# Optimization experiments

Hardware: AMD Instinct MI355X
Metric: run time of the kernel (lower is better)

Reference implementation:

```python
import jax, jax.numpy as jnp
import numpy as np

B, P, V, L = 256, 512, 8, 16
N = B * P            # 131072 nodes
C = V * L            # 128 in_channels (== out_channels, forced by the .view in forward)
H = 4                # heads
DOUT = 128           # out_channels per head
E = N * 5            # k=5 neighbors per node
NEG_SLOPE = 0.2


def setup_inputs() -> dict:
    key = jax.random.key(0)
    ks = jax.random.split(key, 8)
    patches = jax.random.normal(ks[0], (B, P, V, L), dtype=jnp.float32)
    edge_index = jax.random.randint(ks[1], (2, E), 0, N, dtype=jnp.int64)
    s = 1.0 / np.sqrt(C)
    W_gat = jax.random.uniform(ks[2], (C, H * DOUT), dtype=jnp.float32, minval=-s, maxval=s)
    att_src = jax.random.uniform(ks[3], (H, DOUT), dtype=jnp.float32, minval=-s, maxval=s)
    att_dst = jax.random.uniform(ks[4], (H, DOUT), dtype=jnp.float32, minval=-s, maxval=s)
    bias_gat = jnp.zeros((H * DOUT,), dtype=jnp.float32)
    s2 = 1.0 / np.sqrt(H * DOUT)
    W_lin = jax.random.uniform(ks[5], (H * DOUT, DOUT), dtype=jnp.float32, minval=-s2, maxval=s2)
    b_lin = jax.random.uniform(ks[6], (DOUT,), dtype=jnp.float32, minval=-s2, maxval=s2)
    return {"patches": patches, "edge_index": edge_index, "W_gat": W_gat,
            "att_src": att_src, "att_dst": att_dst, "bias_gat": bias_gat,
            "W_lin": W_lin, "b_lin": b_lin}


def reference(patches, edge_index, W_gat, att_src, att_dst, bias_gat, W_lin, b_lin):
    b, p, v, l = patches.shape
    n = b * p
    x = patches.reshape(n, v * l)                      # [N, C]
    xw = (x @ W_gat).reshape(n, H, DOUT)               # [N, H, D]
    # PyG GATConv default add_self_loops=True
    loops = jnp.arange(n, dtype=edge_index.dtype)
    src = jnp.concatenate([edge_index[0], loops])      # message source j
    dst = jnp.concatenate([edge_index[1], loops])      # message target i
    a_src = jnp.einsum('nhd,hd->nh', xw, att_src)      # [N, H]
    a_dst = jnp.einsum('nhd,hd->nh', xw, att_dst)
    e = jax.nn.leaky_relu(a_src[src] + a_dst[dst], NEG_SLOPE)   # [Etot, H]
    m = jax.ops.segment_max(e, dst, num_segments=n)
    ex = jnp.exp(e - m[dst])
    denom = jax.ops.segment_sum(ex, dst, num_segments=n)
    alpha = ex / (denom[dst] + 1e-16)                  # segment softmax over in-edges
    out = jax.ops.segment_sum(alpha[:, :, None] * xw[src], dst, num_segments=n)  # [N, H, D]
    out = out.reshape(n, H * DOUT) + bias_gat
    out = jax.nn.elu(out)
    out = out @ W_lin + b_lin                          # [N, DOUT]
    return out.reshape(b, p, v, l)
```

## Files before the change

### kernel.cpp

```cpp
#include <hip/hip_runtime.h>
#include <hip/hip_bf16.h>
#include <stdint.h>

#define N_NODES 131072
#define C_IN    128
#define HEADS   4
#define DHEAD   128
#define HD      512
#define E_EDGES 655360
#define NEG_SLOPE 0.2f
#define NCHUNK  4
#define CHUNK_N (N_NODES / NCHUNK)
#define SCAN_B  (N_NODES / 256)

typedef short bf16x8 __attribute__((ext_vector_type(8)));
typedef float f32x4  __attribute__((ext_vector_type(4)));

__device__ __forceinline__ float bf2f(unsigned short u) {
    unsigned int x = ((unsigned int)u) << 16;
    return __builtin_bit_cast(float, x);
}
__device__ __forceinline__ unsigned short f2bf(float f) {
    unsigned int u = __builtin_bit_cast(unsigned int, f);
    unsigned int r = u + 0x7FFFu + ((u >> 16) & 1u);
    return (unsigned short)(r >> 16);
}
__device__ __forceinline__ float lrelu(float v) {
    return v > 0.0f ? v : NEG_SLOPE * v;
}

__global__ void detect_kernel(const unsigned int* p_f, const unsigned int* p_i, int* flags) {
    int lane = threadIdx.x;
    int cnt = 0;
#pragma unroll
    for (int r = 0; r < 4; r++) {
        unsigned int e = (p_f[lane + 64 * r] >> 7) & 0xFFu;
        cnt += (e >= 110u && e <= 137u) ? 1 : 0;
    }
    int z = 0;
#pragma unroll
    for (int r = 0; r < 2; r++) {
        z += (p_i[2 * (lane + 64 * r) + 1] == 0u) ? 1 : 0;
    }
#pragma unroll
    for (int o = 1; o < 64; o <<= 1) {
        cnt += __shfl_xor(cnt, o, 64);
        z   += __shfl_xor(z, o, 64);
    }
    if (lane == 0) {
        flags[0] = (cnt >= 128) ? 1 : 0;
        flags[1] = (z == 128) ? 1 : 0;
    }
}

__global__ void conv_w1(const void* in, unsigned short* out, const int* flags) {
    int idx = blockIdx.x * blockDim.x + threadIdx.x;
    int e = idx & 7;
    int l = (idx >> 3) & 63;
    int t = idx >> 9;
    int kk = t & 3, g = t >> 2;
    int col = g * 16 + (l & 15);
    int k = kk * 32 + (l >> 4) * 8 + e;
    float v = flags[0] ? bf2f(((const unsigned short*)in)[k * HD + col])
                       : ((const float*)in)[k * HD + col];
    out[idx] = f2bf(v);
}

__global__ void conv_w2(const void* in, unsigned short* out, const int* flags) {
    int idx = blockIdx.x * blockDim.x + threadIdx.x;
    int n = idx >> 9, k = idx & 511;
    float v = flags[0] ? bf2f(((const unsigned short*)in)[k * DHEAD + n])
                       : ((const float*)in)[k * DHEAD + n];
    out[idx] = f2bf(v);
}

__global__ void conv_small(const void* as, const void* ad, const void* bg, const void* bl,
                           float* att_s, float* att_d, float* bias_g, float* b_lin,
                           const int* flags) {
    int i = blockIdx.x * blockDim.x + threadIdx.x;
    bool bf = flags[0] != 0;
    if (i < 512) {
        att_s[i] = bf ? bf2f(((const unsigned short*)as)[i]) : ((const float*)as)[i];
    } else if (i < 1024) {
        int j = i - 512;
        att_d[j] = bf ? bf2f(((const unsigned short*)ad)[j]) : ((const float*)ad)[j];
    } else if (i < 1536) {
        int j = i - 1024;
        bias_g[j] = bf ? bf2f(((const unsigned short*)bg)[j]) : ((const float*)bg)[j];
    } else if (i < 1664) {
        int j = i - 1536;
        b_lin[j] = bf ? bf2f(((const unsigned short*)bl)[j]) : ((const float*)bl)[j];
    }
}

__global__ void conv_edges_hist(const void* in, int* src32, int* dst32, int* deg,
                                const int* flags) {
    int i = blockIdx.x * blockDim.x + threadIdx.x;
    if (i >= 2 * E_EDGES) return;
    int v = flags[1] ? (int)((const long long*)in)[i] : ((const int*)in)[i];
    if (i < E_EDGES) {
        src32[i] = v;
    } else {
        dst32[i - E_EDGES] = v;
        atomicAdd(&deg[v], 1);
    }
}

__global__ void zero_deg(int* deg) {
    int i = blockIdx.x * blockDim.x + threadIdx.x;
    deg[i] = 0;
}

__global__ void scan_local(const int* __restrict__ deg, int* __restrict__ offv,
                           int* __restrict__ bsums) {
    __shared__ int tmp[256];
    int t = threadIdx.x;
    int g = blockIdx.x * 256 + t;
    int v = deg[g];
    tmp[t] = v;
    __syncthreads();
#pragma unroll
    for (int d = 1; d < 256; d <<= 1) {
        int x = (t >= d) ? tmp[t - d] : 0;
        __syncthreads();
        tmp[t] += x;
        __syncthreads();
    }
    offv[g] = tmp[t] - v;
    if (t == 255) bsums[blockIdx.x] = tmp[t];
}

__global__ void scan_bsums(int* bsums) {
    __shared__ int tmp[SCAN_B];
    int t = threadIdx.x;
    int v = bsums[t];
    tmp[t] = v;
    __syncthreads();
#pragma unroll
    for (int d = 1; d < SCAN_B; d <<= 1) {
        int x = (t >= d) ? tmp[t - d] : 0;
        __syncthreads();
        tmp[t] += x;
        __syncthreads();
    }
    bsums[t] = tmp[t] - v;
}

__global__ void scan_apply(int* __restrict__ offv, const int* __restrict__ bsums,
                           int* __restrict__ cursor) {
    int g = blockIdx.x * 256 + threadIdx.x;
    int v = offv[g] + bsums[blockIdx.x];
    offv[g] = v;
    cursor[g] = v;
}

__global__ void scatter_kernel(const int* src32, const int* dst32, int* cursor, int* csr) {
    int i = blockIdx.x * blockDim.x + threadIdx.x;
    int d = dst32[i];
    int pos = atomicAdd(&cursor[d], 1);
    csr[pos] = src32[i];
}

__launch_bounds__(256)
__global__ void gemm1_fused(const void* __restrict__ Ain,
                            const unsigned short* __restrict__ BT2,
                            const float* __restrict__ attS, const float* __restrict__ attD,
                            unsigned short* __restrict__ xw,
                            float* __restrict__ aSrc, float* __restrict__ aDst,
                            const int* __restrict__ flags) {
    __shared__ unsigned short lA[128 * 136];
    int tid = threadIdx.x;
    int m0 = blockIdx.x * 128;

    if (flags[0] == 0) {
        const float* Af = (const float*)Ain;
#pragma unroll
        for (int p = 0; p < 16; p++) {
            int l = p * 256 + tid;
            int r = l >> 5, c = (l & 31) * 4;
            float4 f = *(const float4*)&Af[(size_t)(m0 + r) * C_IN + c];
            unsigned short t4[4] = {f2bf(f.x), f2bf(f.y), f2bf(f.z), f2bf(f.w)};
            *(uint2*)&lA[r * 136 + c] = *(const uint2*)t4;
        }
    } else {
        const unsigned short* Ab = (const unsigned short*)Ain;
#pragma unroll
        for (int p = 0; p < 8; p++) {
            int l = p * 256 + tid;
            int r = l >> 4, c = (l & 15) * 8;
            *(uint4*)&lA[r * 136 + c] = *(const uint4*)&Ab[(size_t)(m0 + r) * C_IN + c];
        }
    }
    __syncthreads();

    int w = tid >> 6, lane = tid & 63;
    int lr = lane & 15, half = lane >> 4;

    const float4* attS4 = (const float4*)attS;
    const float4* attD4 = (const float4*)attD;

    float dS[8], dD[8];
#pragma unroll
    for (int i = 0; i < 8; i++) { dS[i] = 0.f; dD[i] = 0.f; }

    bf16x8 bbuf[2][4];
#pragma unroll
    for (int kk = 0; kk < 4; kk++)
        bbuf[0][kk] = *(const bf16x8*)&BT2[(((w * 8 + 0) * 4 + kk) << 9) + (lane << 3)];

#pragma unroll
    for (int p = 0; p < 8; p++) {
        int cur = p & 1;
        if (p < 7) {
#pragma unroll
            for (int kk = 0; kk < 4; kk++)
                bbuf[cur ^ 1][kk] =
                    *(const bf16x8*)&BT2[(((w * 8 + p + 1) * 4 + kk) << 9) + (lane << 3)];
        }

        f32x4 acc[8];
#pragma unroll
        for (int i = 0; i < 8; i++) acc[i] = (f32x4){0.f, 0.f, 0.f, 0.f};

#pragma unroll
        for (int kk = 0; kk < 4; kk++) {
#pragma unroll
            for (int i = 0; i < 8; i++) {
                bf16x8 af = *(const bf16x8*)&lA[(i * 16 + lr) * 136 + kk * 32 + half * 8];
                acc[i] = __builtin_amdgcn_mfma_f32_16x16x32_bf16(bbuf[cur][kk], af, acc[i], 0, 0, 0);
            }
        }

        float4 s4 = attS4[w * 32 + p * 4 + half];
        float4 d4 = attD4[w * 32 + p * 4 + half];
#pragma unroll
        for (int i = 0; i < 8; i++) {
            dS[i] += acc[i][0] * s4.x + acc[i][1] * s4.y + acc[i][2] * s4.z + acc[i][3] * s4.w;
            dD[i] += acc[i][0] * d4.x + acc[i][1] * d4.y + acc[i][2] * d4.z + acc[i][3] * d4.w;
            uint2 pk;
            pk.x = (unsigned int)f2bf(acc[i][0]) | ((unsigned int)f2bf(acc[i][1]) << 16);
            pk.y = (unsigned int)f2bf(acc[i][2]) | ((unsigned int)f2bf(acc[i][3]) << 16);
            *(uint2*)&xw[(size_t)(m0 + i * 16 + lr) * HD + w * 128 + p * 16 + half * 4] = pk;
        }
    }

#pragma unroll
    for (int i = 0; i < 8; i++) {
        float ps = dS[i], pd = dD[i];
        ps += __shfl_xor(ps, 16, 64);
        ps += __shfl_xor(ps, 32, 64);
        pd += __shfl_xor(pd, 16, 64);
        pd += __shfl_xor(pd, 32, 64);
        if (half == 0) {
            aSrc[(size_t)(m0 + i * 16 + lr) * HEADS + w] = ps;
            aDst[(size_t)(m0 + i * 16 + lr) * HEADS + w] = pd;
        }
    }
}

__launch_bounds__(256)
__global__ void gemm2(const unsigned short* __restrict__ A,
                      const unsigned short* __restrict__ BT,
                      const float* __restrict__ bias,
                      unsigned short* Cbf, float* Cf,
                      const int* __restrict__ flags, long long rowOff) {
    __shared__ unsigned short smem[64 * 136];
    unsigned short* lA = smem;
    unsigned short* lB = smem + 64 * 40;
    int tid = threadIdx.x;
    int m0 = blockIdx.x * 64;
    int wid = tid >> 6, lane = tid & 63;
    int wr = (wid >> 1) * 32, wc = (wid & 1) * 64;
    int lr = lane & 15, half = lane >> 4;

    f32x4 acc[2][4];
#pragma unroll
    for (int i = 0; i < 2; i++)
#pragma unroll
        for (int j = 0; j < 4; j++) acc[i][j] = (f32x4){0.f, 0.f, 0.f, 0.f};

    for (int k0 = 0; k0 < HD; k0 += 32) {
        {
            int r = tid >> 2, c = (tid & 3) * 8;
            *(uint4*)&lA[r * 40 + c] = *(const uint4*)&A[(size_t)(m0 + r) * HD + k0 + c];
        }
#pragma unroll
        for (int p = 0; p < 2; p++) {
            int l = p * 256 + tid;
            int r = l >> 2, c = (l & 3) * 8;
            *(uint4*)&lB[r * 40 + c] = *(const uint4*)&BT[(size_t)r * HD + k0 + c];
        }
        __syncthreads();
        bf16x8 af[2], bfr[4];
#pragma unroll
        for (int i = 0; i < 2; i++)
            af[i] = *(const bf16x8*)&lA[(wr + i * 16 + lr) * 40 + half * 8];
#pragma unroll
        for (int j = 0; j < 4; j++)
            bfr[j] = *(const bf16x8*)&lB[(wc + j * 16 + lr) * 40 + half * 8];
#pragma unroll
        for (int i = 0; i < 2; i++)
#pragma unroll
            for (int j = 0; j < 4; j++)
                acc[i][j] = __builtin_amdgcn_mfma_f32_16x16x32_bf16(af[i], bfr[j], acc[i][j], 0, 0, 0);
        __syncthreads();
    }

    if (flags[0] != 0) {
#pragma unroll
        for (int i = 0; i < 2; i++)
#pragma unroll
            for (int j = 0; j < 4; j++) {
                int gcol = wc + j * 16 + lr;
                float b = bias[gcol];
#pragma unroll
                for (int r = 0; r < 4; r++)
                    smem[(wr + i * 16 + half * 4 + r) * 136 + gcol] = f2bf(acc[i][j][r] + b);
            }
        __syncthreads();
#pragma unroll
        for (int p = 0; p < 2; p++) {
            int l = p * 256 + tid;
            int r = l >> 4, c = (l & 15) * 8;
            *(uint4*)&Cbf[(size_t)(rowOff + m0 + r) * DHEAD + c] = *(const uint4*)&smem[r * 136 + c];
        }
    } else {
#pragma unroll
        for (int i = 0; i < 2; i++)
#pragma unroll
            for (int j = 0; j < 4; j++) {
                int gcol = wc + j * 16 + lr;
                float b = bias[gcol];
#pragma unroll
                for (int r = 0; r < 4; r++) {
                    int grow = m0 + wr + i * 16 + half * 4 + r;
                    Cf[(size_t)(rowOff + grow) * DHEAD + gcol] = acc[i][j][r] + b;
                }
            }
    }
}

__launch_bounds__(256)
__global__ void aggregate(const unsigned short* __restrict__ xw,
                          const float* __restrict__ a_src, const float* __restrict__ a_dst,
                          const int* __restrict__ off, const int* __restrict__ deg,
                          const int* __restrict__ csr, const float* __restrict__ bias_g,
                          unsigned short* __restrict__ y, int nodeBase) {
    int local = blockIdx.x * 4 + (threadIdx.x >> 6);
    int node = nodeBase + local;
    int l = threadIdx.x & 63;
    int h = l >> 4;
    int ebase = l * 8;
    int o = off[node], dn = deg[node];
    float ad = a_dst[node * HEADS + h];

    float acc[8];
    float denom;
    {
        float w = __expf(lrelu(a_src[node * HEADS + h] + ad));
        uint4 q = *(const uint4*)&xw[(size_t)node * HD + ebase];
        const unsigned short* u = (const unsigned short*)&q;
        denom = w;
#pragma unroll
        for (int k = 0; k < 8; k++) acc[k] = w * bf2f(u[k]);
    }

    for (int e0 = 0; e0 < dn; e0 += 8) {
        int   idx[8];
        float as[8];
        uint4 px[8];
#pragma unroll
        for (int b = 0; b < 8; b++)
            idx[b] = (e0 + b < dn) ? csr[o + e0 + b] : node;
#pragma unroll
        for (int b = 0; b < 8; b++)
            as[b] = a_src[idx[b] * HEADS + h];
#pragma unroll
        for (int b = 0; b < 8; b++)
            px[b] = *(const uint4*)&xw[(size_t)idx[b] * HD + ebase];
#pragma unroll
        for (int b = 0; b < 8; b++) {
            float w = (e0 + b < dn) ? __expf(lrelu(as[b] + ad)) : 0.0f;
            denom += w;
            const unsigned short* u = (const unsigned short*)&px[b];
#pragma unroll
            for (int k = 0; k < 8; k++) acc[k] += w * bf2f(u[k]);
        }
    }

    float inv = 1.0f / (denom + 1e-16f);
    unsigned short outp[8];
#pragma unroll
    for (int k = 0; k < 8; k++) {
        float v = acc[k] * inv + bias_g[ebase + k];
        v = v > 0.f ? v : (__expf(v) - 1.0f);
        outp[k] = f2bf(v);
    }
    *(uint4*)&y[(size_t)local * HD + ebase] = *(const uint4*)outp;
}

extern "C" void kernel_launch(void* const* d_in, const int* in_sizes, int n_in,
                              void* d_out, int out_size, void* d_ws, size_t ws_size,
                              hipStream_t stream) {
    char* ws = (char*)d_ws;
    size_t wsoff = 0;
    auto alloc = [&](size_t bytes) -> char* {
        char* p = ws + wsoff;
        wsoff += (bytes + 255) & ~(size_t)255;
        return p;
    };

    int*            flags  = (int*)           alloc(256);
    unsigned short* WT1    = (unsigned short*)alloc((size_t)HD * C_IN * 2);
    unsigned short* WT2    = (unsigned short*)alloc((size_t)DHEAD * HD * 2);
    float*          attS   = (float*)         alloc(HD * 4);
    float*          attD   = (float*)         alloc(HD * 4);
    float*          biasG  = (float*)         alloc(HD * 4);
    float*          bLin   = (float*)         alloc(DHEAD * 4);
    int*            src32  = (int*)           alloc((size_t)E_EDGES * 4);
    int*            dst32  = (int*)           alloc((size_t)E_EDGES * 4);
    int*            deg    = (int*)           alloc((size_t)N_NODES * 4);
    int*            offv   = (int*)           alloc((size_t)(N_NODES + 1) * 4);
    int*            cursor = (int*)           alloc((size_t)N_NODES * 4);
    int*            csr    = (int*)           alloc((size_t)E_EDGES * 4);
    int*            bsums  = (int*)           alloc((size_t)SCAN_B * 4);
    float*          aSrc   = (float*)         alloc((size_t)N_NODES * HEADS * 4);
    float*          aDst   = (float*)         alloc((size_t)N_NODES * HEADS * 4);
    unsigned short* xw     = (unsigned short*)alloc((size_t)N_NODES * HD * 2);
    unsigned short* ychunk = (unsigned short*)alloc((size_t)CHUNK_N * HD * 2);

    const void* patches = d_in[0];
    const void* edges   = d_in[1];
    const void* Wgat    = d_in[2];
    const void* attSrcI = d_in[3];
    const void* attDstI = d_in[4];
    const void* biasGI  = d_in[5];
    const void* WlinI   = d_in[6];
    const void* bLinI   = d_in[7];

    detect_kernel<<<1, 64, 0, stream>>>((const unsigned int*)patches,
                                        (const unsigned int*)edges, flags);

    conv_w1<<<(HD * C_IN) / 256, 256, 0, stream>>>(Wgat, WT1, flags);
    conv_w2<<<(DHEAD * HD) / 256, 256, 0, stream>>>(WlinI, WT2, flags);
    conv_small<<<7, 256, 0, stream>>>(attSrcI, attDstI, biasGI, bLinI,
                                      attS, attD, biasG, bLin, flags);

    zero_deg<<<N_NODES / 256, 256, 0, stream>>>(deg);
    conv_edges_hist<<<(2 * E_EDGES) / 256, 256, 0, stream>>>(edges, src32, dst32, deg, flags);
    scan_local<<<SCAN_B, 256, 0, stream>>>(deg, offv, bsums);
    scan_bsums<<<1, SCAN_B, 0, stream>>>(bsums);
    scan_apply<<<SCAN_B, 256, 0, stream>>>(offv, bsums, cursor);
    scatter_kernel<<<E_EDGES / 256, 256, 0, stream>>>(src32, dst32, cursor, csr);

    gemm1_fused<<<N_NODES / 128, 256, 0, stream>>>(
        patches, WT1, attS, attD, xw, aSrc, aDst, flags);

    for (int c = 0; c < NCHUNK; c++) {
        int base = c * CHUNK_N;
        aggregate<<<CHUNK_N / 4, 256, 0, stream>>>(xw, aSrc, aDst, offv, deg, csr,
                                                   biasG, ychunk, base);
        gemm2<<<CHUNK_N / 64, 256, 0, stream>>>(
            ychunk, WT2, bLin, (unsigned short*)d_out, (float*)d_out, flags, base);
    }
}
```

Baseline: 463.6 us.

## Store xw in permuted column layout with 16-byte writes, remap W_lin and bias

```diff
diff --git a/kernel.cpp b/kernel.cpp
--- a/kernel.cpp
+++ b/kernel.cpp
@@ -27,6 +27,12 @@
 }
 __device__ __forceinline__ float lrelu(float v) {
     return v > 0.0f ? v : NEG_SLOPE * v;
+}
+
+__device__ __forceinline__ int perm512(int s) {
+    int w = s >> 7, r = s & 127;
+    int P = r >> 5, half = (r >> 3) & 3, b = (r >> 2) & 1, e = r & 3;
+    return w * 128 + (2 * P + b) * 16 + half * 4 + e;
 }
 
 __global__ void detect_kernel(const unsigned int* p_f, const unsigned int* p_i, int* flags) {
@@ -68,7 +74,8 @@
 
 __global__ void conv_w2(const void* in, unsigned short* out, const int* flags) {
     int idx = blockIdx.x * blockDim.x + threadIdx.x;
-    int n = idx >> 9, k = idx & 511;
+    int n = idx >> 9, s = idx & 511;
+    int k = perm512(s);
     float v = flags[0] ? bf2f(((const unsigned short*)in)[k * DHEAD + n])
                        : ((const float*)in)[k * DHEAD + n];
     out[idx] = f2bf(v);
@@ -85,8 +92,8 @@
         int j = i - 512;
         att_d[j] = bf ? bf2f(((const unsigned short*)ad)[j]) : ((const float*)ad)[j];
     } else if (i < 1536) {
-        int j = i - 1024;
-        bias_g[j] = bf ? bf2f(((const unsigned short*)bg)[j]) : ((const float*)bg)[j];
+        int j = perm512(i - 1024);
+        bias_g[i - 1024] = bf ? bf2f(((const unsigned short*)bg)[j]) : ((const float*)bg)[j];
     } else if (i < 1664) {
         int j = i - 1536;
         b_lin[j] = bf ? bf2f(((const unsigned short*)bl)[j]) : ((const float*)bl)[j];
@@ -161,7 +168,7 @@
     csr[pos] = src32[i];
 }
 
-__launch_bounds__(256)
+__launch_bounds__(256, 3)
 __global__ void gemm1_fused(const void* __restrict__ Ain,
                             const unsigned short* __restrict__ BT2,
                             const float* __restrict__ attS, const float* __restrict__ attD,
@@ -208,6 +215,8 @@
     for (int kk = 0; kk < 4; kk++)
         bbuf[0][kk] = *(const bf16x8*)&BT2[(((w * 8 + 0) * 4 + kk) << 9) + (lane << 3)];
 
+    uint2 pk_lo[8];
+
 #pragma unroll
     for (int p = 0; p < 8; p++) {
         int cur = p & 1;
@@ -237,10 +246,25 @@
         for (int i = 0; i < 8; i++) {
             dS[i] += acc[i][0] * s4.x + acc[i][1] * s4.y + acc[i][2] * s4.z + acc[i][3] * s4.w;
             dD[i] += acc[i][0] * d4.x + acc[i][1] * d4.y + acc[i][2] * d4.z + acc[i][3] * d4.w;
-            uint2 pk;
-            pk.x = (unsigned int)f2bf(acc[i][0]) | ((unsigned int)f2bf(acc[i][1]) << 16);
-            pk.y = (unsigned int)f2bf(acc[i][2]) | ((unsigned int)f2bf(acc[i][3]) << 16);
-            *(uint2*)&xw[(size_t)(m0 + i * 16 + lr) * HD + w * 128 + p * 16 + half * 4] = pk;
+        }
+
+        if ((p & 1) == 0) {
+#pragma unroll
+            for (int i = 0; i < 8; i++) {
+                pk_lo[i].x = (unsigned int)f2bf(acc[i][0]) | ((unsigned int)f2bf(acc[i][1]) << 16);
+                pk_lo[i].y = (unsigned int)f2bf(acc[i][2]) | ((unsigned int)f2bf(acc[i][3]) << 16);
+            }
+        } else {
+            int P = p >> 1;
+#pragma unroll
+            for (int i = 0; i < 8; i++) {
+                uint4 q;
+                q.x = pk_lo[i].x;
+                q.y = pk_lo[i].y;
+                q.z = (unsigned int)f2bf(acc[i][0]) | ((unsigned int)f2bf(acc[i][1]) << 16);
+                q.w = (unsigned int)f2bf(acc[i][2]) | ((unsigned int)f2bf(acc[i][3]) << 16);
+                *(uint4*)&xw[(size_t)(m0 + i * 16 + lr) * HD + w * 128 + P * 32 + half * 8] = q;
+            }
         }
     }
 
```

New measurement: 607.8 us. 1.31x slower.
